# Performance work log

Hardware: AMD Instinct MI355X
Metric: run time of the kernel (lower is better)

The kernel has to match this reference:

```python
import jax, jax.numpy as jnp
import numpy as np

N = 100000; E = 1000000; D = 192; FD = 64; L = 6; MLP = 192
TW = 768; NPD = 6; CPD = 7; TEMP = 0.5; NREL = 2; EPS = 1e-5


def _ln(x, g, b):
    mu = jnp.mean(x, axis=-1, keepdims=True)
    var = jnp.mean(jnp.square(x - mu), axis=-1, keepdims=True)
    return (x - mu) * jax.lax.rsqrt(var + EPS) * g + b


def _bn(x, g, b):
    # BatchNorm1d in training mode: batch statistics over the N (node) axis
    mu = jnp.mean(x, axis=0, keepdims=True)
    var = jnp.mean(jnp.square(x - mu), axis=0, keepdims=True)
    return (x - mu) * jax.lax.rsqrt(var + EPS) * g + b


def _rgcn(x, Wrel, Wroot, bias, src, dst, etype):
    # PyG RGCNConv, aggr='mean': out_i = x_i @ Wroot + b + sum_r mean_{j in N_r(i)} x_j @ W_r
    out = x @ Wroot + bias
    for r in range(NREL):
        h = x @ Wrel[r]                                   # [N, D] per-relation transform
        mask = (etype == r)
        msg = jnp.where(mask[:, None], jnp.take(h, src, axis=0), 0.0)  # [E, D]
        agg = jax.ops.segment_sum(msg, dst, num_segments=N)
        cnt = jax.ops.segment_sum(mask.astype(x.dtype), dst, num_segments=N)
        out = out + agg / jnp.maximum(cnt, 1.0)[:, None]
    return out


def _forward(tweet, num_prop, comments_prop,
             Wt, bt, Wn, bnum, Wc, bc,
             Wv, bv, Wo, bo, ln1_g, ln1_b, bn_g, bn_b,
             W1, b1, W2, b2, ln2_g, ln2_b,
             Wrel, Wroot, rgcn_b, Wm1, bm1, Wm2, bm2, Wm3, bm3,
             edge_index, edge_type, labels, train_idx):
    lrelu = jax.nn.leaky_relu  # negative_slope=0.01, same as torch LeakyReLU default
    t = lrelu(tweet @ Wt + bt)
    n = lrelu(num_prop @ Wn + bnum)
    c = lrelu(comments_prop @ Wc + bc)
    x = jnp.concatenate([t, n, c], axis=1)  # [N, D]; seq dim of size 1 is elided
    for i in range(L):
        # MHA over seq_len=1: softmax over a single key is exactly 1, so
        # attn_out = out_proj(v_proj(x)); Q/K projections have zero effect/grad.
        v = x @ Wv[i] + bv[i]
        x = x + (v @ Wo[i] + bo[i])          # dropout in eval mode = identity
        x = _ln(x, ln1_g[i], ln1_b[i])
        x = _bn(x, bn_g[i], bn_b[i])
        f = lrelu(x @ W1[i] + b1[i]) @ W2[i] + b2[i]
        x = x + f
        x = _ln(x, ln2_g[i], ln2_b[i])
    # supervised contrastive loss on first train_idx nodes (train_idx static int)
    feat = x[:train_idx]
    lab = labels[:train_idx]
    fn = feat / jnp.linalg.norm(feat, axis=-1, keepdims=True)
    sim = (fn @ fn.T) / TEMP                              # [T, T]
    ex = jnp.exp(sim)
    match = (lab[:, None] == lab[None, :]).astype(x.dtype)
    closs = jnp.mean(-jnp.log(jnp.sum(match * ex, axis=1) / jnp.sum(ex, axis=1)))
    # two passes through the SAME (shared-weight) RGCN; dropout(p=0.1) eval = identity
    src, dst = edge_index[0], edge_index[1]
    h = _rgcn(x, Wrel, Wroot, rgcn_b, src, dst, edge_type)
    h = _rgcn(h, Wrel, Wroot, rgcn_b, src, dst, edge_type)
    h = lrelu(h @ Wm1 + bm1)
    h = lrelu(h @ Wm2 + bm2)
    logits = h @ Wm3 + bm3                                # [N, 2]
    return logits, closs


def setup_inputs() -> dict:
    key = jax.random.key(0)
    ks = iter(jax.random.split(key, 64))
    f32 = jnp.float32
    def p(*shape):
        fan_in = shape[-2] if len(shape) >= 2 else shape[-1]
        return jax.random.normal(next(ks), shape, f32) * (1.0 / np.sqrt(fan_in))
    inp = {
        'tweet': jax.random.normal(next(ks), (N, TW), f32),
        'num_prop': jax.random.normal(next(ks), (N, NPD), f32),
        'comments_prop': jax.random.normal(next(ks), (N, CPD), f32),
        'Wt': p(TW, FD), 'bt': jnp.zeros((FD,), f32),
        'Wn': p(NPD, FD), 'bnum': jnp.zeros((FD,), f32),
        'Wc': p(CPD, FD), 'bc': jnp.zeros((FD,), f32),
        'Wv': p(L, D, D), 'bv': jnp.zeros((L, D), f32),
        'Wo': p(L, D, D), 'bo': jnp.zeros((L, D), f32),
        'ln1_g': jnp.ones((L, D), f32), 'ln1_b': jnp.zeros((L, D), f32),
        'bn_g': jnp.ones((L, D), f32), 'bn_b': jnp.zeros((L, D), f32),
        'W1': p(L, D, MLP), 'b1': jnp.zeros((L, MLP), f32),
        'W2': p(L, MLP, D), 'b2': jnp.zeros((L, D), f32),
        'ln2_g': jnp.ones((L, D), f32), 'ln2_b': jnp.zeros((L, D), f32),
        'Wrel': p(NREL, D, D), 'Wroot': p(D, D), 'rgcn_b': jnp.zeros((D,), f32),
        'Wm1': p(D, MLP), 'bm1': jnp.zeros((MLP,), f32),
        'Wm2': p(MLP, D), 'bm2': jnp.zeros((D,), f32),
        'Wm3': p(D, 2), 'bm3': jnp.zeros((2,), f32),
        'edge_index': jax.random.randint(next(ks), (2, E), 0, N, jnp.int32),
        'edge_type': jax.random.randint(next(ks), (E,), 0, NREL, jnp.int32),
        'labels': jax.random.randint(next(ks), (N,), 0, 2, jnp.int32),
        'train_idx': 8192,
    }
    return inp


def reference(tweet, num_prop, comments_prop, Wt, bt, Wn, bnum, Wc, bc,
              Wv, bv, Wo, bo, ln1_g, ln1_b, bn_g, bn_b,
              W1, b1, W2, b2, ln2_g, ln2_b,
              Wrel, Wroot, rgcn_b, Wm1, bm1, Wm2, bm2, Wm3, bm3,
              edge_index, edge_type, labels, train_idx):
    return _forward(tweet, num_prop, comments_prop, Wt, bt, Wn, bnum, Wc, bc,
                    Wv, bv, Wo, bo, ln1_g, ln1_b, bn_g, bn_b,
                    W1, b1, W2, b2, ln2_g, ln2_b,
                    Wrel, Wroot, rgcn_b, Wm1, bm1, Wm2, bm2, Wm3, bm3,
                    edge_index, edge_type, labels, train_idx)
```

## Files before the change

### kernel.cpp

```cpp
#include <hip/hip_runtime.h>

#define NN 100000
#define EE 1000000
#define DDIM 192
#define NLAYER 6
#define TRAIN 8192
#define SLOPE 0.01f
#define EPS_LN 1e-5f
#define TOTSEG (2 * NN)
#define SCAN_NB 98

typedef float f32x4 __attribute__((ext_vector_type(4)));
typedef __bf16 bf16x8 __attribute__((ext_vector_type(8)));
typedef unsigned short ushort_t;
typedef unsigned int uint_t;

__device__ __forceinline__ float lrelu(float v) { return v > 0.0f ? v : SLOPE * v; }

__device__ __forceinline__ ushort_t f2bf(float f) {
    __bf16 h = (__bf16)f;
    return __builtin_bit_cast(ushort_t, h);
}

__device__ __forceinline__ float bf2f(ushort_t b) {
// ... 12 lines not shown
    const float* __restrict__ W2, const float* __restrict__ Wrel,
    const float* __restrict__ Wroot, const float* __restrict__ Wm1,
    const float* __restrict__ Wm2, ushort_t* __restrict__ WTt,
    ushort_t* __restrict__ WTs, ushort_t* __restrict__ WTg)
{
    const int bid = blockIdx.x;
    if (bid < 29 * 144) {
        const int mat = bid / 144;
        const int o = (bid % 144) * 256 + threadIdx.x;
        const float* src;
        if      (mat <  6) src = Wv   + (size_t)mat * 36864;
        else if (mat < 12) src = Wo   + (size_t)(mat - 6)  * 36864;
        else if (mat < 18) src = W1   + (size_t)(mat - 12) * 36864;
        else if (mat < 24) src = W2   + (size_t)(mat - 18) * 36864;
        else if (mat < 26) src = Wrel + (size_t)(mat - 24) * 36864;
        else if (mat == 26) src = Wroot;
        else if (mat == 27) src = Wm1;
        else                src = Wm2;
        const int m = o / 192, k = o - m * 192;
        const ushort_t b = f2bf(src[(size_t)k * 192 + m]);
        if (mat == 24 || mat == 25)
            WTg[(size_t)m * 576 + 192 + (mat - 24) * 192 + k] = b;
        else if (mat == 26)
            WTg[(size_t)m * 576 + k] = b;
        else
            WTs[(size_t)mat * 36864 + o] = b;
    } else {
        const int o = (bid - 29 * 144) * 256 + threadIdx.x;
        const int m = o / 768, k = o - m * 768;
        WTt[o] = f2bf(Wt[(size_t)k * 64 + m]);
    }
}

template <int NFRAG, bool BIAS, bool RELU>
__global__ __launch_bounds__(256) void gemm_mfma(
    const float* __restrict__ A, const ushort_t* __restrict__ WT,
    const float* __restrict__ bias, float* __restrict__ C,
    int n, int K, int ldc)
{
    __shared__ ushort_t As[128 * 32];
    __shared__ ushort_t Ws[NFRAG * 16 * 32];
    const int tid = threadIdx.x;
    const int lane = tid & 63, w = tid >> 6;
    const int quad = lane >> 4, l15 = lane & 15;
    const int row0 = blockIdx.x * 128;

    f32x4 acc[2][NFRAG];
    #pragma unroll
    for (int m = 0; m < 2; ++m)
        #pragma unroll
        for (int nf = 0; nf < NFRAG; ++nf)
            acc[m][nf] = (f32x4){0.f, 0.f, 0.f, 0.f};

    const int srow = tid >> 1, shalf = tid & 1;
    const bool arow_ok = (row0 + srow) < n;
    const float* aptr = A + (size_t)(row0 + srow) * K + shalf * 16;
    const int ktiles = K >> 5;

    float f[16];
    if (arow_ok) {
        const float4* p = (const float4*)aptr;
        #pragma unroll
        for (int i = 0; i < 4; ++i) {
            const float4 t4 = p[i];
            f[i * 4 + 0] = t4.x; f[i * 4 + 1] = t4.y;
            f[i * 4 + 2] = t4.z; f[i * 4 + 3] = t4.w;
        }
    } else {
        #pragma unroll
        for (int i = 0; i < 16; ++i) f[i] = 0.f;
    }

    for (int t = 0; t < ktiles; ++t) {
        const int k0 = t << 5;
        uint_t u[8];
        #pragma unroll
        for (int i = 0; i < 8; ++i)
            u[i] = (uint_t)f2bf(f[2 * i]) | ((uint_t)f2bf(f[2 * i + 1]) << 16);
        uint4* dsta = (uint4*)&As[srow * 32 + shalf * 16];
        dsta[0] = make_uint4(u[0], u[1], u[2], u[3]);
        dsta[1] = make_uint4(u[4], u[5], u[6], u[7]);

        #pragma unroll
        for (int s = tid; s < NFRAG * 64; s += 256) {
            const int col = s >> 2, part = s & 3;
            *(uint4*)&Ws[col * 32 + part * 8] =
                *(const uint4*)(WT + (size_t)col * K + k0 + part * 8);
        }
        __syncthreads();

        float fn_[16];
        const bool more = (t + 1 < ktiles);
        if (more) {
            if (arow_ok) {
                const float4* p = (const float4*)(aptr + k0 + 32);
                #pragma unroll
                for (int i = 0; i < 4; ++i) {
                    const float4 t4 = p[i];
                    fn_[i * 4 + 0] = t4.x; fn_[i * 4 + 1] = t4.y;
                    fn_[i * 4 + 2] = t4.z; fn_[i * 4 + 3] = t4.w;
                }
            } else {
                #pragma unroll
                for (int i = 0; i < 16; ++i) fn_[i] = 0.f;
            }
        }

        const bf16x8 a0 = *(const bf16x8*)&As[(w * 32 + l15) * 32 + quad * 8];
        const bf16x8 a1 = *(const bf16x8*)&As[(w * 32 + 16 + l15) * 32 + quad * 8];
        #pragma unroll
        for (int nf = 0; nf < NFRAG; ++nf) {
            const bf16x8 b = *(const bf16x8*)&Ws[(nf * 16 + l15) * 32 + quad * 8];
            acc[0][nf] = __builtin_amdgcn_mfma_f32_16x16x32_bf16(a0, b, acc[0][nf], 0, 0, 0);
            acc[1][nf] = __builtin_amdgcn_mfma_f32_16x16x32_bf16(a1, b, acc[1][nf], 0, 0, 0);
        }
        __syncthreads();
        if (more) {
            #pragma unroll
            for (int i = 0; i < 16; ++i) f[i] = fn_[i];
        }
    }

    #pragma unroll
    for (int m = 0; m < 2; ++m) {
        #pragma unroll
        for (int reg = 0; reg < 4; ++reg) {
            const int gr = row0 + w * 32 + m * 16 + quad * 4 + reg;
            if (gr >= n) continue;
            #pragma unroll
            for (int nf = 0; nf < NFRAG; ++nf) {
                const int col = nf * 16 + l15;
                float x = acc[m][nf][reg] + (BIAS ? bias[col] : 0.f);
                if (RELU) x = lrelu(x);
                C[(size_t)gr * ldc + col] = x;
            }
        }
    }
}

template <bool ABF, bool RELU1, bool RELU2, bool RES, bool LNORM, bool BN,
          bool BNSTAT, bool CF32, bool CBF>
__global__ __launch_bounds__(512, 4) void gemm2_mfma(
    const void* __restrict__ Ain, const ushort_t* __restrict__ wta,
    const float* __restrict__ bias1, const ushort_t* __restrict__ wtb,
    const float* __restrict__ bias2, const void* __restrict__ resin,
    float* __restrict__ C, ushort_t* __restrict__ Cbf,
    const float* __restrict__ bnsum, const float* __restrict__ bng,
    const float* __restrict__ bnb, float* __restrict__ bnacc,
    const float* __restrict__ lg, const float* __restrict__ lb, int n)
{
    constexpr int VST = 200;
    __shared__ ushort_t Vs[128 * VST];
    __shared__ ushort_t Ws[2][192 * 32];
    __shared__ float scs[DDIM], shs[DDIM];
    const int tid = threadIdx.x;
    const int lane = tid & 63, w = tid >> 6;
    const int quad = lane >> 4, l15 = lane & 15;
    const int row0 = blockIdx.x * 128;
    const int myrow = row0 + w * 16 + l15;
    const bool rok = myrow < n;

    if constexpr (BN) {
        const float invN = 1.0f / (float)NN;
        for (int j = tid; j < DDIM; j += 512) {
            const float mu = bnsum[j] * invN;
            const float var = bnsum[DDIM + j] * invN - mu * mu;
            const float sc = bng[j] * rsqrtf(var + EPS_LN);
            scs[j] = sc;
            shs[j] = fmaf(-mu, sc, bnb[j]);
        }
    }

    f32x4 acc[12];
    #pragma unroll
    for (int nf = 0; nf < 12; ++nf) acc[nf] = (f32x4){0.f, 0.f, 0.f, 0.f};

    const float*    aF = (const float*)Ain    + (size_t)myrow * DDIM + quad * 8;
    const ushort_t* aB = (const ushort_t*)Ain + (size_t)myrow * DDIM + quad * 8;

    auto stageW = [&](const ushort_t* wt, int t, int b) {
        const int k0 = t << 5;
        for (int s = tid; s < 768; s += 512) {
            const int col = s >> 2, part = s & 3;
            *(uint4*)&Ws[b][col * 32 + part * 8] =
                *(const uint4*)(wt + (size_t)col * DDIM + k0 + part * 8);
        }
    };
    auto loadA = [&](int t, float* fo, uint4& uo) {
        if constexpr (!ABF) {
            if (rok) {
                const float4 p0 = *(const float4*)(aF + t * 32);
                const float4 p1 = *(const float4*)(aF + t * 32 + 4);
                fo[0] = p0.x; fo[1] = p0.y; fo[2] = p0.z; fo[3] = p0.w;
                fo[4] = p1.x; fo[5] = p1.y; fo[6] = p1.z; fo[7] = p1.w;
            } else {
                #pragma unroll
                for (int i = 0; i < 8; ++i) fo[i] = 0.f;
            }
        } else {
            uo = rok ? *(const uint4*)(aB + t * 32) : make_uint4(0u, 0u, 0u, 0u);
        }
    };
    auto makeA = [&](const float* fi, const uint4& ui, int t) -> bf16x8 {
        if constexpr (!ABF) {
            union { uint_t u[4]; bf16x8 v; } r;
            #pragma unroll
            for (int i = 0; i < 4; ++i)
                r.u[i] = (uint_t)f2bf(fi[2 * i]) | ((uint_t)f2bf(fi[2 * i + 1]) << 16);
            return r.v;
        } else if constexpr (BN) {
            const int c0 = (t << 5) + quad * 8;
            const float4 sc0 = *(const float4*)&scs[c0];
            const float4 sc1 = *(const float4*)&scs[c0 + 4];
            const float4 sh0 = *(const float4*)&shs[c0];
            const float4 sh1 = *(const float4*)&shs[c0 + 4];
            const uint_t* uw = (const uint_t*)&ui;
            float x[8];
            #pragma unroll
            for (int i = 0; i < 4; ++i) {
                x[2 * i]     = bf2f((ushort_t)(uw[i] & 0xffffu));
                x[2 * i + 1] = bf2f((ushort_t)(uw[i] >> 16));
            }
            x[0] = fmaf(x[0], sc0.x, sh0.x); x[1] = fmaf(x[1], sc0.y, sh0.y);
            x[2] = fmaf(x[2], sc0.z, sh0.z); x[3] = fmaf(x[3], sc0.w, sh0.w);
            x[4] = fmaf(x[4], sc1.x, sh1.x); x[5] = fmaf(x[5], sc1.y, sh1.y);
            x[6] = fmaf(x[6], sc1.z, sh1.z); x[7] = fmaf(x[7], sc1.w, sh1.w);
            union { uint_t u[4]; bf16x8 v; } r;
            #pragma unroll
            for (int i = 0; i < 4; ++i)
                r.u[i] = (uint_t)f2bf(x[2 * i]) | ((uint_t)f2bf(x[2 * i + 1]) << 16);
            return r.v;
        } else {
            return __builtin_bit_cast(bf16x8, ui);
        }
    };

    float fc[8]; uint4 uc;
    stageW(wta, 0, 0);
    loadA(0, fc, uc);
    __syncthreads();
    #pragma unroll 2
    for (int t = 0; t < 6; ++t) {
        const int b = t & 1;
        if (t < 5) stageW(wta, t + 1, b ^ 1);
        float fn[8]; uint4 un;
        if (t < 5) loadA(t + 1, fn, un);
        const bf16x8 a = makeA(fc, uc, t);
        #pragma unroll
        for (int nf = 0; nf < 12; ++nf) {
            const bf16x8 bb = *(const bf16x8*)&Ws[b][(nf * 16 + l15) * 32 + quad * 8];
            acc[nf] = __builtin_amdgcn_mfma_f32_16x16x32_bf16(a, bb, acc[nf], 0, 0, 0);
        }
        __syncthreads();
        if (t < 5) {
            if constexpr (!ABF) {
                #pragma unroll
                for (int i = 0; i < 8; ++i) fc[i] = fn[i];
            } else uc = un;
        }
    }

    {
        float b1r[12];
        #pragma unroll
        for (int nf = 0; nf < 12; ++nf) b1r[nf] = bias1[nf * 16 + l15];
        #pragma unroll
        for (int reg = 0; reg < 4; ++reg) {
            ushort_t* vrow = &Vs[(w * 16 + quad * 4 + reg) * VST + l15];
            #pragma unroll
            for (int nf = 0; nf < 12; ++nf) {
                float x = acc[nf][reg] + b1r[nf];
                if (RELU1) x = lrelu(x);
                vrow[nf * 16] = f2bf(x);
                acc[nf][reg] = 0.f;
            }
        }
    }
    stageW(wtb, 0, 0);
    __syncthreads();

    #pragma unroll 2
    for (int t = 0; t < 6; ++t) {
        const int b = t & 1;
        if (t < 5) stageW(wtb, t + 1, b ^ 1);
        const bf16x8 a = *(const bf16x8*)&Vs[(w * 16 + l15) * VST + (t << 5) + quad * 8];
        #pragma unroll
        for (int nf = 0; nf < 12; ++nf) {
            const bf16x8 bb = *(const bf16x8*)&Ws[b][(nf * 16 + l15) * 32 + quad * 8];
            acc[nf] = __builtin_amdgcn_mfma_f32_16x16x32_bf16(a, bb, acc[nf], 0, 0, 0);
        }
        __syncthreads();
    }

    int   col[12];
    float bia[12];
    #pragma unroll
    for (int nf = 0; nf < 12; ++nf) {
        col[nf] = nf * 16 + l15;
        bia[nf] = bias2[col[nf]];
    }
    float rsc[12], rsh[12];
    if constexpr (BN && RES) {
        #pragma unroll
        for (int nf = 0; nf < 12; ++nf) {
            rsc[nf] = scs[col[nf]];
            rsh[nf] = shs[col[nf]];
        }
    }
    float cs[12], cs2[12];
    if constexpr (BNSTAT) {
        #pragma unroll
        for (int nf = 0; nf < 12; ++nf) { cs[nf] = 0.f; cs2[nf] = 0.f; }
    }
    #pragma unroll
    for (int reg = 0; reg < 4; ++reg) {
        const int gr = row0 + w * 16 + quad * 4 + reg;
        const bool ok = gr < n;
        float v[12];
        #pragma unroll
        for (int nf = 0; nf < 12; ++nf) {
            float x = acc[nf][reg] + bia[nf];
            if constexpr (RES) {
                float r;
                if constexpr (ABF)
                    r = ok ? bf2f(((const ushort_t*)resin)[(size_t)gr * DDIM + col[nf]]) : 0.f;
                else
                    r = ok ? ((const float*)resin)[(size_t)gr * DDIM + col[nf]] : 0.f;
                if constexpr (BN) r = fmaf(r, rsc[nf], rsh[nf]);
                x += r;
            }
            v[nf] = x;
        }
        if constexpr (LNORM) {
            float s = 0.f, s2 = 0.f;
            #pragma unroll
            for (int nf = 0; nf < 12; ++nf) { s += v[nf]; s2 = fmaf(v[nf], v[nf], s2); }
            #pragma unroll
            for (int off = 1; off < 16; off <<= 1) {
                s  += __shfl_xor(s, off);
                s2 += __shfl_xor(s2, off);
            }
            const float mu = s * (1.0f / DDIM);
            const float var = s2 * (1.0f / DDIM) - mu * mu;
            const float rs = rsqrtf(var + EPS_LN);
            #pragma unroll
            for (int nf = 0; nf < 12; ++nf)
                v[nf] = fmaf((v[nf] - mu) * rs, lg[col[nf]], lb[col[nf]]);
        }
        #pragma unroll
        for (int nf = 0; nf < 12; ++nf) {
            float x = v[nf];
            if (RELU2) x = lrelu(x);
            if constexpr (BNSTAT) {
                const float xa = ok ? x : 0.f;
                cs[nf] += xa;
                cs2[nf] = fmaf(xa, xa, cs2[nf]);
            }
            if (ok) {
                if constexpr (CF32) C[(size_t)gr * DDIM + col[nf]] = x;
                if constexpr (CBF)  Cbf[(size_t)gr * DDIM + col[nf]] = f2bf(x);
            }
        }
    }
    if constexpr (BNSTAT) {
        float* bsA = (float*)&Ws[0][0];
        float* bsB = bsA + 8 * 192;
        #pragma unroll
        for (int nf = 0; nf < 12; ++nf) {
            cs[nf]  += __shfl_xor(cs[nf], 16);  cs[nf]  += __shfl_xor(cs[nf], 32);
            cs2[nf] += __shfl_xor(cs2[nf], 16); cs2[nf] += __shfl_xor(cs2[nf], 32);
        }
        if (quad == 0) {
            #pragma unroll
            for (int nf = 0; nf < 12; ++nf) {
                bsA[w * 192 + col[nf]] = cs[nf];
                bsB[w * 192 + col[nf]] = cs2[nf];
            }
        }
        __syncthreads();
        if (tid < DDIM) {
            float s = 0.f, s2 = 0.f;
            #pragma unroll
            for (int k = 0; k < 8; ++k) {
                s  += bsA[k * 192 + tid];
                s2 += bsB[k * 192 + tid];
            }
            atomicAdd(&bnacc[tid], s);
            atomicAdd(&bnacc[DDIM + tid], s2);
        }
    }
}

__global__ __launch_bounds__(512, 4) void gemm_cat(
// ... 37 lines not shown

    #pragma unroll 2
    for (int t = 0; t < 18; ++t) {
        const int b = t & 1;
        if (t < 17) stageW(t + 1, b ^ 1);
        uint4 un;
        if (t < 17) un = loadA(t + 1);
        const bf16x8 a = __builtin_bit_cast(bf16x8, uc);
        #pragma unroll
        for (int nf = 0; nf < 12; ++nf) {
            const bf16x8 bb = *(const bf16x8*)&Ws[b][(nf * 16 + l15) * 32 + quad * 8];
            acc[nf] = __builtin_amdgcn_mfma_f32_16x16x32_bf16(a, bb, acc[nf], 0, 0, 0);
        }
        __syncthreads();
        if (t < 17) uc = un;
    }

    #pragma unroll
    for (int reg = 0; reg < 4; ++reg) {
        const int gr = row0 + w * 16 + quad * 4 + reg;
        if (gr >= n) continue;
        #pragma unroll
        for (int nf = 0; nf < 12; ++nf) {
            const int col = nf * 16 + l15;
            Cbf[(size_t)gr * DDIM + col] = f2bf(acc[nf][reg] + bias[col]);
        }
    }
}

__global__ __launch_bounds__(256) void embed_nc_k(
    const float* __restrict__ np_, const float* __restrict__ cp,
    const float* __restrict__ Wn, const float* __restrict__ bnum,
    const float* __restrict__ Wc, const float* __restrict__ bc,
    float* __restrict__ x)
{
    const int idx = blockIdx.x * 256 + threadIdx.x;
    if (idx >= NN * 128) return;
    const int node = idx >> 7;
    const int c = idx & 127;
    float acc;
    if (c < 64) {
        acc = bnum[c];
        #pragma unroll
        for (int k = 0; k < 6; ++k) acc = fmaf(np_[node * 6 + k], Wn[k * 64 + c], acc);
    } else {
        const int cc = c - 64;
        acc = bc[cc];
        #pragma unroll
        for (int k = 0; k < 7; ++k) acc = fmaf(cp[node * 7 + k], Wc[k * 64 + cc], acc);
    }
    x[(size_t)node * DDIM + 64 + c] = lrelu(acc);
}

__global__ __launch_bounds__(256) void fnorm_k(const float* __restrict__ x,
                                               ushort_t* __restrict__ fnb)
{
    const int wave = threadIdx.x >> 6, lane = threadIdx.x & 63;
    const int row = blockIdx.x * 4 + wave;
    if (row >= TRAIN) return;
    const float* xr = x + (size_t)row * DDIM;
    const float v0 = xr[lane], v1 = xr[lane + 64], v2 = xr[lane + 128];
    const float q = wave_sum(v0 * v0 + v1 * v1 + v2 * v2);
    const float inv = 1.0f / sqrtf(q);
    ushort_t* fr = fnb + (size_t)row * DDIM;
    fr[lane]       = f2bf(v0 * inv);
    fr[lane + 64]  = f2bf(v1 * inv);
    fr[lane + 128] = f2bf(v2 * inv);
}

__global__ __launch_bounds__(256) void sim_mfma(const ushort_t* __restrict__ fnb,
    const int* __restrict__ lab, float* __restrict__ row_ex, float* __restrict__ row_mt)
{
    __shared__ ushort_t Ai[128 * 32];
    __shared__ ushort_t Bj[128 * 32];
    __shared__ int Li[128], Lj[128];
    const int tid = threadIdx.x, lane = tid & 63, w = tid >> 6;
    const int quad = lane >> 4, l15 = lane & 15;
    const int i0 = blockIdx.x * 128, j0 = blockIdx.y * 128;
    if (tid < 128) Li[tid] = lab[i0 + tid];
    else           Lj[tid - 128] = lab[j0 + tid - 128];
    const int iw = (w >> 1) * 64, jw = (w & 1) * 64;

    f32x4 acc[4][4];
    #pragma unroll
    for (int m = 0; m < 4; ++m)
        #pragma unroll
        for (int nf = 0; nf < 4; ++nf)
            acc[m][nf] = (f32x4){0.f, 0.f, 0.f, 0.f};

    for (int k0 = 0; k0 < DDIM; k0 += 32) {
        #pragma unroll
        for (int s = tid; s < 512; s += 256) {
            const int row = s >> 2, part = s & 3;
            *(uint4*)&Ai[row * 32 + part * 8] =
                *(const uint4*)(fnb + (size_t)(i0 + row) * DDIM + k0 + part * 8);
            *(uint4*)&Bj[row * 32 + part * 8] =
                *(const uint4*)(fnb + (size_t)(j0 + row) * DDIM + k0 + part * 8);
        }
        __syncthreads();
        bf16x8 a[4], b[4];
        #pragma unroll
        for (int m = 0; m < 4; ++m)
            a[m] = *(const bf16x8*)&Ai[(iw + m * 16 + l15) * 32 + quad * 8];
        #pragma unroll
        for (int nf = 0; nf < 4; ++nf)
            b[nf] = *(const bf16x8*)&Bj[(jw + nf * 16 + l15) * 32 + quad * 8];
        #pragma unroll
        for (int m = 0; m < 4; ++m)
            #pragma unroll
            for (int nf = 0; nf < 4; ++nf)
                acc[m][nf] = __builtin_amdgcn_mfma_f32_16x16x32_bf16(a[m], b[nf], acc[m][nf], 0, 0, 0);
        __syncthreads();
    }

    int lj[4];
    #pragma unroll
    for (int nf = 0; nf < 4; ++nf) lj[nf] = Lj[jw + nf * 16 + l15];
    #pragma unroll
    for (int m = 0; m < 4; ++m) {
        #pragma unroll
        for (int reg = 0; reg < 4; ++reg) {
            const int rl = iw + m * 16 + quad * 4 + reg;
            const int li = Li[rl];
            float se = 0.f, sm = 0.f;
            #pragma unroll
            for (int nf = 0; nf < 4; ++nf) {
                const float e = __expf(acc[m][nf][reg] * 2.0f);
                se += e;
                if (li == lj[nf]) sm += e;
            }
            #pragma unroll
            for (int off = 1; off < 16; off <<= 1) {
                se += __shfl_xor(se, off);
                sm += __shfl_xor(sm, off);
            }
            if (l15 == 0) {
                atomicAdd(&row_ex[i0 + rl], se);
                atomicAdd(&row_mt[i0 + rl], sm);
            }
        }
    }
}

__global__ __launch_bounds__(256) void closs_k(const float* __restrict__ ex,
    const float* __restrict__ mt, float* __restrict__ out)
{
    float s = 0.f;
    for (int i = threadIdx.x; i < TRAIN; i += 256) s += -logf(mt[i] / ex[i]);
    s = wave_sum(s);
    __shared__ float red[4];
    const int wave = threadIdx.x >> 6, lane = threadIdx.x & 63;
    if (lane == 0) red[wave] = s;
    __syncthreads();
    if (threadIdx.x == 0) out[0] = (red[0] + red[1] + red[2] + red[3]) / (float)TRAIN;
}

__global__ __launch_bounds__(256) void cnt_i_k(const int* __restrict__ dst,
    const int* __restrict__ ety, int* __restrict__ cnti)
{
    const int e = blockIdx.x * 256 + threadIdx.x;
    if (e >= EE) return;
    atomicAdd(&cnti[(size_t)ety[e] * NN + dst[e]], 1);
}

__global__ __launch_bounds__(256) void part_k(const int* __restrict__ cnti,
                                              int* __restrict__ part)
{
    __shared__ int sh[256];
    const int tid = threadIdx.x;
    const int i0 = blockIdx.x * 2048 + tid * 8;
    int s = 0;
// ... 84 lines not shown
        const int seg = r * NN + d;
        const int end = offs[seg];
        const int c = cnti[seg];
        float a0 = 0.f, a1 = 0.f, b0 = 0.f, b1 = 0.f;
        int e = end - c;
        for (; e + 1 < end; e += 2) {
            const int s0 = elist[e], s1 = elist[e + 1];
            const uint_t* r0 = (const uint_t*)(xb + (size_t)s0 * DDIM);
            const uint_t* r1 = (const uint_t*)(xb + (size_t)s1 * DDIM);
            const uint_t x0 = r0[lane], x1 = r1[lane];
            uint_t y0 = 0u, y1 = 0u;
            if (lo) { y0 = r0[64 + lane]; y1 = r1[64 + lane]; }
            a0 += bf2f((ushort_t)(x0 & 0xffffu)) + bf2f((ushort_t)(x1 & 0xffffu));
            a1 += bf2f((ushort_t)(x0 >> 16))     + bf2f((ushort_t)(x1 >> 16));
            b0 += bf2f((ushort_t)(y0 & 0xffffu)) + bf2f((ushort_t)(y1 & 0xffffu));
            b1 += bf2f((ushort_t)(y0 >> 16))     + bf2f((ushort_t)(y1 >> 16));
        }
        if (e < end) {
            const int s0 = elist[e];
            const uint_t* r0 = (const uint_t*)(xb + (size_t)s0 * DDIM);
            const uint_t x0 = r0[lane];
            uint_t y0 = 0u;
            if (lo) y0 = r0[64 + lane];
            a0 += bf2f((ushort_t)(x0 & 0xffffu));
            a1 += bf2f((ushort_t)(x0 >> 16));
            b0 += bf2f((ushort_t)(y0 & 0xffffu));
            b1 += bf2f((ushort_t)(y0 >> 16));
        }
        const float inv = 1.0f / (float)max(c, 1);
        uint_t* ar = (uint_t*)(aggb + (size_t)d * 384 + r * DDIM);
        ar[lane] = (uint_t)f2bf(a0 * inv) | ((uint_t)f2bf(a1 * inv) << 16);
        if (lo)
            ar[64 + lane] = (uint_t)f2bf(b0 * inv) | ((uint_t)f2bf(b1 * inv) << 16);
    }
}

__global__ __launch_bounds__(256) void logits_k(const float* __restrict__ h,
    const float* __restrict__ Wm3, const float* __restrict__ bm3, float* __restrict__ out)
{
    const int wave = threadIdx.x >> 6, lane = threadIdx.x & 63;
    const int row = blockIdx.x * 4 + wave;
    if (row >= NN) return;
    const float* hr = h + (size_t)row * DDIM;
    float s0 = 0.f, s1 = 0.f;
    #pragma unroll
    for (int p = 0; p < 3; ++p) {
        const int k = lane + p * 64;
        const float v = hr[k];
        s0 = fmaf(v, Wm3[k * 2 + 0], s0);
        s1 = fmaf(v, Wm3[k * 2 + 1], s1);
    }
    #pragma unroll
    for (int off = 32; off > 0; off >>= 1) {
        s0 += __shfl_down(s0, off);
        s1 += __shfl_down(s1, off);
    }
    if (lane == 0) {
        out[(size_t)row * 2 + 0] = s0 + bm3[0];
        out[(size_t)row * 2 + 1] = s1 + bm3[1];
    }
}

extern "C" void kernel_launch(void* const* d_in, const int* in_sizes, int n_in,
                              void* d_out, int out_size, void* d_ws, size_t ws_size,
                              hipStream_t stream)
{
    const float* tweet   = (const float*)d_in[0];
    const float* np_     = (const float*)d_in[1];
    const float* cp      = (const float*)d_in[2];
    const float* Wt      = (const float*)d_in[3];
    const float* bt      = (const float*)d_in[4];
    const float* Wn      = (const float*)d_in[5];
    const float* bnum    = (const float*)d_in[6];
    const float* Wc      = (const float*)d_in[7];
    const float* bc      = (const float*)d_in[8];
    const float* Wv      = (const float*)d_in[9];
    const float* bv      = (const float*)d_in[10];
    const float* Wo      = (const float*)d_in[11];
    const float* bo      = (const float*)d_in[12];
    const float* ln1g    = (const float*)d_in[13];
    const float* ln1b    = (const float*)d_in[14];
    const float* bng     = (const float*)d_in[15];
    const float* bnb     = (const float*)d_in[16];
    const float* W1      = (const float*)d_in[17];
    const float* b1      = (const float*)d_in[18];
    const float* W2      = (const float*)d_in[19];
    const float* b2      = (const float*)d_in[20];
    const float* ln2g    = (const float*)d_in[21];
    const float* ln2b    = (const float*)d_in[22];
    const float* Wrel    = (const float*)d_in[23];
    const float* Wroot   = (const float*)d_in[24];
    const float* rgcnb   = (const float*)d_in[25];
    const float* Wm1     = (const float*)d_in[26];
    const float* bm1     = (const float*)d_in[27];
    const float* Wm2     = (const float*)d_in[28];
    const float* bm2     = (const float*)d_in[29];
    const float* Wm3     = (const float*)d_in[30];
    const float* bm3     = (const float*)d_in[31];
    const int*   eidx    = (const int*)d_in[32];
    const int*   esrc    = eidx;
    const int*   edst    = eidx + EE;
    const int*   ety     = (const int*)d_in[33];
    const int*   labels  = (const int*)d_in[34];
    float* out = (float*)d_out;

    float* ws = (float*)d_ws;
    const size_t ND = (size_t)NN * DDIM;
    float* B0    = ws;
    float* B1    = B0 + ND;
    float* B2    = B1 + ND;
    float* B3    = B2 + ND;
    float* ROWEX = B3 + ND;
    float* ROWMT = ROWEX + TRAIN;
    float* BNS   = ROWMT + TRAIN;
    int*   CNTI  = (int*)(BNS + 12 * DDIM);
    int*   OFFS  = CNTI + 2 * NN;
    int*   ELIST = OFFS + 2 * NN;
    int*   PART  = ELIST + EE;
    ushort_t* FNb = (ushort_t*)(PART + 128);
    ushort_t* WTt = FNb + (size_t)TRAIN * DDIM;
    ushort_t* WTs = WTt + 49152;
    ushort_t* WTv    = WTs;
    ushort_t* WTo    = WTs + (size_t)6  * 36864;
    ushort_t* WT1    = WTs + (size_t)12 * 36864;
    ushort_t* WT2    = WTs + (size_t)18 * 36864;
    ushort_t* WTm1   = WTs + (size_t)27 * 36864;
    ushort_t* WTm2   = WTs + (size_t)28 * 36864;
    ushort_t* XBF  = (ushort_t*)B3;
    ushort_t* WTg  = (ushort_t*)B3 + ND;
    ushort_t* X1BF = (ushort_t*)B2;
    ushort_t* AGGB = (ushort_t*)B2;

    const int gx = (NN + 127) / 128;
    const dim3 blk(256);
    const dim3 blk5(512);

    prep_w<<<29 * 144 + 192, blk, 0, stream>>>(Wt, Wv, Wo, W1, W2, Wrel, Wroot, Wm1, Wm2, WTt, WTs, WTg);

    hipMemsetAsync(CNTI, 0, 2 * NN * sizeof(int), stream);
    cnt_i_k<<<(EE + 255) / 256, blk, 0, stream>>>(edst, ety, CNTI);
    part_k<<<SCAN_NB, blk, 0, stream>>>(CNTI, PART);
    scanp_k<<<1, 128, 0, stream>>>(PART);
    offs_k<<<SCAN_NB, blk, 0, stream>>>(CNTI, PART, OFFS);
    fill_k<<<(EE + 255) / 256, blk, 0, stream>>>(esrc, edst, ety, OFFS, ELIST);

    gemm_mfma<4, true, true><<<gx, blk, 0, stream>>>(tweet, WTt, bt, B0, NN, 768, DDIM);
    embed_nc_k<<<(NN * 128 + 255) / 256, blk, 0, stream>>>(np_, cp, Wn, bnum, Wc, bc, B0);

    hipMemsetAsync(BNS, 0, 12 * DDIM * sizeof(float), stream);
    for (int i = 0; i < NLAYER; ++i) {
        const size_t wo = (size_t)i * 36864;
        float* bnacc_i = BNS + (size_t)i * 2 * DDIM;
        gemm2_mfma<false, false, false, true, true, false, true, false, true>
            <<<gx, blk5, 0, stream>>>(
            B0, WTv + wo, bv + i * DDIM, WTo + wo, bo + i * DDIM, B0,
            nullptr, X1BF, nullptr, nullptr, nullptr, bnacc_i,
            ln1g + i * DDIM, ln1b + i * DDIM, NN);
        if (i < NLAYER - 1)
            gemm2_mfma<true, true, false, true, true, true, false, true, false>
                <<<gx, blk5, 0, stream>>>(
                X1BF, WT1 + wo, b1 + i * DDIM, WT2 + wo, b2 + i * DDIM, X1BF,
                B0, nullptr, bnacc_i, bng + i * DDIM, bnb + i * DDIM, nullptr,
                ln2g + i * DDIM, ln2b + i * DDIM, NN);
        else
            gemm2_mfma<true, true, false, true, true, true, false, true, true>
                <<<gx, blk5, 0, stream>>>(
                X1BF, WT1 + wo, b1 + i * DDIM, WT2 + wo, b2 + i * DDIM, X1BF,
                B0, XBF, bnacc_i, bng + i * DDIM, bnb + i * DDIM, nullptr,
                ln2g + i * DDIM, ln2b + i * DDIM, NN);
    }

    hipMemsetAsync(ROWEX, 0, 2 * TRAIN * sizeof(float), stream);
    fnorm_k<<<TRAIN / 4, blk, 0, stream>>>(B0, FNb);
    sim_mfma<<<dim3(TRAIN / 128, TRAIN / 128), blk, 0, stream>>>(FNb, labels, ROWEX, ROWMT);
    closs_k<<<1, blk, 0, stream>>>(ROWEX, ROWMT, out + 2 * (size_t)NN);

    gather_bf_k<<<(NN + 3) / 4, blk, 0, stream>>>(XBF, ELIST, OFFS, CNTI, AGGB);
    gemm_cat<<<gx, blk5, 0, stream>>>(XBF, AGGB, WTg, rgcnb, XBF, NN);

    gather_bf_k<<<(NN + 3) / 4, blk, 0, stream>>>(XBF, ELIST, OFFS, CNTI, AGGB);
    gemm_cat<<<gx, blk5, 0, stream>>>(XBF, AGGB, WTg, rgcnb, XBF, NN);

    gemm2_mfma<true, true, true, false, false, false, false, true, false>
        <<<gx, blk5, 0, stream>>>(
        XBF, WTm1, bm1, WTm2, bm2, nullptr, B2, nullptr,
        nullptr, nullptr, nullptr, nullptr, nullptr, nullptr, NN);
    logits_k<<<(NN + 3) / 4, blk, 0, stream>>>(B2, Wm3, bm3, out);
}
```

Baseline: 1.894 ms.

## Store activations in bf16 and fuse logits, fnorm, and symmetric similarity

The residual stream is now kept entirely in bf16: the tweet embedding GEMM and the layer GEMMs write bf16 instead of fp32, which roughly halves activation traffic. The logits head is fused into the final MLP GEMM epilogue, and feature normalisation is fused into the last layer's epilogue. The similarity kernel now computes only the lower-triangular tiles and adds each off-diagonal tile's contributions to both rows and columns, halving its MFMA work at the cost of extra atomics. The tweet GEMM is rewritten with 512 threads and a double-buffered weight tile. Keeping the residual in bf16 adds rounding error at every layer.

New measurement: 1.852 ms. 1.02x faster.

```diff
diff --git a/kernel.cpp b/kernel.cpp
--- a/kernel.cpp
+++ b/kernel.cpp
@@ -68,122 +68,93 @@
     }
 }
 
-template <int NFRAG, bool BIAS, bool RELU>
-__global__ __launch_bounds__(256) void gemm_mfma(
+__global__ __launch_bounds__(512) void gemm_tweet(
     const float* __restrict__ A, const ushort_t* __restrict__ WT,
-    const float* __restrict__ bias, float* __restrict__ C,
-    int n, int K, int ldc)
-{
-    __shared__ ushort_t As[128 * 32];
-    __shared__ ushort_t Ws[NFRAG * 16 * 32];
+    const float* __restrict__ bias, ushort_t* __restrict__ Cbf, int n)
+{
+    __shared__ ushort_t Ws[2][64 * 32];
     const int tid = threadIdx.x;
     const int lane = tid & 63, w = tid >> 6;
     const int quad = lane >> 4, l15 = lane & 15;
     const int row0 = blockIdx.x * 128;
-
-    f32x4 acc[2][NFRAG];
-    #pragma unroll
-    for (int m = 0; m < 2; ++m)
-        #pragma unroll
-        for (int nf = 0; nf < NFRAG; ++nf)
-            acc[m][nf] = (f32x4){0.f, 0.f, 0.f, 0.f};
-
-    const int srow = tid >> 1, shalf = tid & 1;
-    const bool arow_ok = (row0 + srow) < n;
-    const float* aptr = A + (size_t)(row0 + srow) * K + shalf * 16;
-    const int ktiles = K >> 5;
-
-    float f[16];
-    if (arow_ok) {
-        const float4* p = (const float4*)aptr;
-        #pragma unroll
-        for (int i = 0; i < 4; ++i) {
-            const float4 t4 = p[i];
-            f[i * 4 + 0] = t4.x; f[i * 4 + 1] = t4.y;
-            f[i * 4 + 2] = t4.z; f[i * 4 + 3] = t4.w;
-        }
-    } else {
-        #pragma unroll
-        for (int i = 0; i < 16; ++i) f[i] = 0.f;
-    }
-
-    for (int t = 0; t < ktiles; ++t) {
-        const int k0 = t << 5;
-        uint_t u[8];
-        #pragma unroll
-        for (int i = 0; i < 8; ++i)
-            u[i] = (uint_t)f2bf(f[2 * i]) | ((uint_t)f2bf(f[2 * i + 1]) << 16);
-        uint4* dsta = (uint4*)&As[srow * 32 + shalf * 16];
-        dsta[0] = make_uint4(u[0], u[1], u[2], u[3]);
-        dsta[1] = make_uint4(u[4], u[5], u[6], u[7]);
-
-        #pragma unroll
-        for (int s = tid; s < NFRAG * 64; s += 256) {
-            const int col = s >> 2, part = s & 3;
-            *(uint4*)&Ws[col * 32 + part * 8] =
-                *(const uint4*)(WT + (size_t)col * K + k0 + part * 8);
-        }
-        __syncthreads();
-
-        float fn_[16];
-        const bool more = (t + 1 < ktiles);
-        if (more) {
-            if (arow_ok) {
-                const float4* p = (const float4*)(aptr + k0 + 32);
-                #pragma unroll
-                for (int i = 0; i < 4; ++i) {
-                    const float4 t4 = p[i];
-                    fn_[i * 4 + 0] = t4.x; fn_[i * 4 + 1] = t4.y;
-                    fn_[i * 4 + 2] = t4.z; fn_[i * 4 + 3] = t4.w;
-                }
-            } else {
-                #pragma unroll
-                for (int i = 0; i < 16; ++i) fn_[i] = 0.f;
-            }
-        }
-
-        const bf16x8 a0 = *(const bf16x8*)&As[(w * 32 + l15) * 32 + quad * 8];
-        const bf16x8 a1 = *(const bf16x8*)&As[(w * 32 + 16 + l15) * 32 + quad * 8];
-        #pragma unroll
-        for (int nf = 0; nf < NFRAG; ++nf) {
-            const bf16x8 b = *(const bf16x8*)&Ws[(nf * 16 + l15) * 32 + quad * 8];
-            acc[0][nf] = __builtin_amdgcn_mfma_f32_16x16x32_bf16(a0, b, acc[0][nf], 0, 0, 0);
-            acc[1][nf] = __builtin_amdgcn_mfma_f32_16x16x32_bf16(a1, b, acc[1][nf], 0, 0, 0);
-        }
-        __syncthreads();
-        if (more) {
-            #pragma unroll
-            for (int i = 0; i < 16; ++i) f[i] = fn_[i];
-        }
-    }
-
-    #pragma unroll
-    for (int m = 0; m < 2; ++m) {
-        #pragma unroll
-        for (int reg = 0; reg < 4; ++reg) {
-            const int gr = row0 + w * 32 + m * 16 + quad * 4 + reg;
-            if (gr >= n) continue;
-            #pragma unroll
-            for (int nf = 0; nf < NFRAG; ++nf) {
-                const int col = nf * 16 + l15;
-                float x = acc[m][nf][reg] + (BIAS ? bias[col] : 0.f);
-                if (RELU) x = lrelu(x);
-                C[(size_t)gr * ldc + col] = x;
-            }
-        }
-    }
-}
-
-template <bool ABF, bool RELU1, bool RELU2, bool RES, bool LNORM, bool BN,
-          bool BNSTAT, bool CF32, bool CBF>
+    const int myrow = row0 + w * 16 + l15;
+    const bool rok = myrow < n;
+
+    f32x4 acc[4];
+    #pragma unroll
+    for (int nf = 0; nf < 4; ++nf) acc[nf] = (f32x4){0.f, 0.f, 0.f, 0.f};
+
+    const float* aF = A + (size_t)myrow * 768 + quad * 8;
+
+    auto stageW = [&](int t, int b) {
+        if (tid < 256) {
+            const int col = tid >> 2, part = tid & 3;
+            *(uint4*)&Ws[b][col * 32 + part * 8] =
+                *(const uint4*)(WT + (size_t)col * 768 + (t << 5) + part * 8);
+        }
+    };
+    auto loadA = [&](int t, float* fo) {
+        if (rok) {
+            const float4 p0 = *(const float4*)(aF + t * 32);
+            const float4 p1 = *(const float4*)(aF + t * 32 + 4);
+            fo[0] = p0.x; fo[1] = p0.y; fo[2] = p0.z; fo[3] = p0.w;
+            fo[4] = p1.x; fo[5] = p1.y; fo[6] = p1.z; fo[7] = p1.w;
+        } else {
+            #pragma unroll
+            for (int i = 0; i < 8; ++i) fo[i] = 0.f;
+        }
+    };
+
+    float fc[8];
+    stageW(0, 0);
+    loadA(0, fc);
+    __syncthreads();
+    #pragma unroll 2
+    for (int t = 0; t < 24; ++t) {
+        const int b = t & 1;
+        if (t < 23) stageW(t + 1, b ^ 1);
+        float fn[8];
+        if (t < 23) loadA(t + 1, fn);
+        union { uint_t u[4]; bf16x8 v; } r;
+        #pragma unroll
+        for (int i = 0; i < 4; ++i)
+            r.u[i] = (uint_t)f2bf(fc[2 * i]) | ((uint_t)f2bf(fc[2 * i + 1]) << 16);
+        #pragma unroll
+        for (int nf = 0; nf < 4; ++nf) {
+            const bf16x8 bb = *(const bf16x8*)&Ws[b][(nf * 16 + l15) * 32 + quad * 8];
+            acc[nf] = __builtin_amdgcn_mfma_f32_16x16x32_bf16(r.v, bb, acc[nf], 0, 0, 0);
+        }
+        __syncthreads();
+        if (t < 23) {
+            #pragma unroll
+            for (int i = 0; i < 8; ++i) fc[i] = fn[i];
+        }
+    }
+
+    #pragma unroll
+    for (int reg = 0; reg < 4; ++reg) {
+        const int gr = row0 + w * 16 + quad * 4 + reg;
+        if (gr >= n) continue;
+        #pragma unroll
+        for (int nf = 0; nf < 4; ++nf) {
+            const int col = nf * 16 + l15;
+            Cbf[(size_t)gr * DDIM + col] = f2bf(lrelu(acc[nf][reg] + bias[col]));
+        }
+    }
+}
+
+template <bool RELU1, bool RELU2, bool RES, bool LNORM, bool BN,
+          bool BNSTAT, bool CBF, bool LOGITS, bool FNORM>
 __global__ __launch_bounds__(512, 4) void gemm2_mfma(
-    const void* __restrict__ Ain, const ushort_t* __restrict__ wta,
+    const ushort_t* __restrict__ Ain, const ushort_t* __restrict__ wta,
     const float* __restrict__ bias1, const ushort_t* __restrict__ wtb,
-    const float* __restrict__ bias2, const void* __restrict__ resin,
-    float* __restrict__ C, ushort_t* __restrict__ Cbf,
+    const float* __restrict__ bias2, const ushort_t* __restrict__ resin,
+    ushort_t* __restrict__ Cbf,
     const float* __restrict__ bnsum, const float* __restrict__ bng,
     const float* __restrict__ bnb, float* __restrict__ bnacc,
-    const float* __restrict__ lg, const float* __restrict__ lb, int n)
+    const float* __restrict__ lg, const float* __restrict__ lb,
+    const float* __restrict__ Wm3, const float* __restrict__ bm3,
+    float* __restrict__ outp, ushort_t* __restrict__ fnb, int n)
 {
     constexpr int VST = 200;
     __shared__ ushort_t Vs[128 * VST];
@@ -211,8 +182,7 @@
     #pragma unroll
     for (int nf = 0; nf < 12; ++nf) acc[nf] = (f32x4){0.f, 0.f, 0.f, 0.f};
 
-    const float*    aF = (const float*)Ain    + (size_t)myrow * DDIM + quad * 8;
-    const ushort_t* aB = (const ushort_t*)Ain + (size_t)myrow * DDIM + quad * 8;
+    const ushort_t* aB = Ain + (size_t)myrow * DDIM + quad * 8;
 
     auto stageW = [&](const ushort_t* wt, int t, int b) {
         const int k0 = t << 5;
@@ -222,29 +192,11 @@
                 *(const uint4*)(wt + (size_t)col * DDIM + k0 + part * 8);
         }
     };
-    auto loadA = [&](int t, float* fo, uint4& uo) {
-        if constexpr (!ABF) {
-            if (rok) {
-                const float4 p0 = *(const float4*)(aF + t * 32);
-                const float4 p1 = *(const float4*)(aF + t * 32 + 4);
-                fo[0] = p0.x; fo[1] = p0.y; fo[2] = p0.z; fo[3] = p0.w;
-                fo[4] = p1.x; fo[5] = p1.y; fo[6] = p1.z; fo[7] = p1.w;
-            } else {
-                #pragma unroll
-                for (int i = 0; i < 8; ++i) fo[i] = 0.f;
-            }
-        } else {
-            uo = rok ? *(const uint4*)(aB + t * 32) : make_uint4(0u, 0u, 0u, 0u);
-        }
+    auto loadA = [&](int t) -> uint4 {
+        return rok ? *(const uint4*)(aB + t * 32) : make_uint4(0u, 0u, 0u, 0u);
     };
-    auto makeA = [&](const float* fi, const uint4& ui, int t) -> bf16x8 {
-        if constexpr (!ABF) {
-            union { uint_t u[4]; bf16x8 v; } r;
-            #pragma unroll
-            for (int i = 0; i < 4; ++i)
-                r.u[i] = (uint_t)f2bf(fi[2 * i]) | ((uint_t)f2bf(fi[2 * i + 1]) << 16);
-            return r.v;
-        } else if constexpr (BN) {
+    auto makeA = [&](const uint4& ui, int t) -> bf16x8 {
+        if constexpr (BN) {
             const int c0 = (t << 5) + quad * 8;
             const float4 sc0 = *(const float4*)&scs[c0];
             const float4 sc1 = *(const float4*)&scs[c0 + 4];
@@ -271,29 +223,24 @@
         }
     };
 
-    float fc[8]; uint4 uc;
+    uint4 uc;
     stageW(wta, 0, 0);
-    loadA(0, fc, uc);
+    uc = loadA(0);
     __syncthreads();
     #pragma unroll 2
     for (int t = 0; t < 6; ++t) {
         const int b = t & 1;
         if (t < 5) stageW(wta, t + 1, b ^ 1);
-        float fn[8]; uint4 un;
-        if (t < 5) loadA(t + 1, fn, un);
-        const bf16x8 a = makeA(fc, uc, t);
+        uint4 un;
+        if (t < 5) un = loadA(t + 1);
+        const bf16x8 a = makeA(uc, t);
         #pragma unroll
         for (int nf = 0; nf < 12; ++nf) {
             const bf16x8 bb = *(const bf16x8*)&Ws[b][(nf * 16 + l15) * 32 + quad * 8];
             acc[nf] = __builtin_amdgcn_mfma_f32_16x16x32_bf16(a, bb, acc[nf], 0, 0, 0);
         }
         __syncthreads();
-        if (t < 5) {
-            if constexpr (!ABF) {
-                #pragma unroll
-                for (int i = 0; i < 8; ++i) fc[i] = fn[i];
-            } else uc = un;
-        }
+        if (t < 5) uc = un;
     }
 
     {
@@ -343,6 +290,14 @@
             rsh[nf] = shs[col[nf]];
         }
     }
+    float w3a[12], w3b[12];
+    if constexpr (LOGITS) {
+        #pragma unroll
+        for (int nf = 0; nf < 12; ++nf) {
+            w3a[nf] = Wm3[col[nf] * 2 + 0];
+            w3b[nf] = Wm3[col[nf] * 2 + 1];
+        }
+    }
     float cs[12], cs2[12];
     if constexpr (BNSTAT) {
         #pragma unroll
@@ -357,11 +312,7 @@
         for (int nf = 0; nf < 12; ++nf) {
             float x = acc[nf][reg] + bia[nf];
             if constexpr (RES) {
-                float r;
-                if constexpr (ABF)
-                    r = ok ? bf2f(((const ushort_t*)resin)[(size_t)gr * DDIM + col[nf]]) : 0.f;
-                else
-                    r = ok ? ((const float*)resin)[(size_t)gr * DDIM + col[nf]] : 0.f;
+                float r = ok ? bf2f(resin[(size_t)gr * DDIM + col[nf]]) : 0.f;
                 if constexpr (BN) r = fmaf(r, rsc[nf], rsh[nf]);
                 x += r;
             }
@@ -383,6 +334,7 @@
             for (int nf = 0; nf < 12; ++nf)
                 v[nf] = fmaf((v[nf] - mu) * rs, lg[col[nf]], lb[col[nf]]);
         }
+        float s0 = 0.f, s1 = 0.f;
         #pragma unroll
         for (int nf = 0; nf < 12; ++nf) {
             float x = v[nf];
@@ -392,9 +344,36 @@
                 cs[nf] += xa;
                 cs2[nf] = fmaf(xa, xa, cs2[nf]);
             }
+            if constexpr (LOGITS) {
+                s0 = fmaf(x, w3a[nf], s0);
+                s1 = fmaf(x, w3b[nf], s1);
+            }
             if (ok) {
-                if constexpr (CF32) C[(size_t)gr * DDIM + col[nf]] = x;
-                if constexpr (CBF)  Cbf[(size_t)gr * DDIM + col[nf]] = f2bf(x);
+                if constexpr (CBF) Cbf[(size_t)gr * DDIM + col[nf]] = f2bf(x);
+            }
+        }
+        if constexpr (LOGITS) {
+            #pragma unroll
+            for (int off = 1; off < 16; off <<= 1) {
+                s0 += __shfl_xor(s0, off);
+                s1 += __shfl_xor(s1, off);
+            }
+            if (l15 == 0 && ok) {
+                outp[(size_t)gr * 2 + 0] = s0 + bm3[0];
+                outp[(size_t)gr * 2 + 1] = s1 + bm3[1];
+            }
+        }
+        if constexpr (FNORM) {
+            if (gr < TRAIN) {
+                float q = 0.f;
+                #pragma unroll
+                for (int nf = 0; nf < 12; ++nf) q = fmaf(v[nf], v[nf], q);
+                #pragma unroll
+                for (int off = 1; off < 16; off <<= 1) q += __shfl_xor(q, off);
+                const float inv = 1.0f / sqrtf(q);
+                #pragma unroll
+                for (int nf = 0; nf < 12; ++nf)
+                    fnb[(size_t)gr * DDIM + col[nf]] = f2bf(v[nf] * inv);
             }
         }
     }
@@ -498,7 +477,7 @@
     const float* __restrict__ np_, const float* __restrict__ cp,
     const float* __restrict__ Wn, const float* __restrict__ bnum,
     const float* __restrict__ Wc, const float* __restrict__ bc,
-    float* __restrict__ x)
+    ushort_t* __restrict__ xb)
 {
     const int idx = blockIdx.x * 256 + threadIdx.x;
     if (idx >= NN * 128) return;
@@ -515,23 +494,7 @@
         #pragma unroll
         for (int k = 0; k < 7; ++k) acc = fmaf(cp[node * 7 + k], Wc[k * 64 + cc], acc);
     }
-    x[(size_t)node * DDIM + 64 + c] = lrelu(acc);
-}
-
-__global__ __launch_bounds__(256) void fnorm_k(const float* __restrict__ x,
-                                               ushort_t* __restrict__ fnb)
-{
-    const int wave = threadIdx.x >> 6, lane = threadIdx.x & 63;
-    const int row = blockIdx.x * 4 + wave;
-    if (row >= TRAIN) return;
-    const float* xr = x + (size_t)row * DDIM;
-    const float v0 = xr[lane], v1 = xr[lane + 64], v2 = xr[lane + 128];
-    const float q = wave_sum(v0 * v0 + v1 * v1 + v2 * v2);
-    const float inv = 1.0f / sqrtf(q);
-    ushort_t* fr = fnb + (size_t)row * DDIM;
-    fr[lane]       = f2bf(v0 * inv);
-    fr[lane + 64]  = f2bf(v1 * inv);
-    fr[lane + 128] = f2bf(v2 * inv);
+    xb[(size_t)node * DDIM + 64 + c] = f2bf(lrelu(acc));
 }
 
 __global__ __launch_bounds__(256) void sim_mfma(const ushort_t* __restrict__ fnb,
@@ -540,9 +503,16 @@
     __shared__ ushort_t Ai[128 * 32];
     __shared__ ushort_t Bj[128 * 32];
     __shared__ int Li[128], Lj[128];
+    const int bid = blockIdx.x;
+    int ti = (int)((sqrtf(8.0f * (float)bid + 1.0f) - 1.0f) * 0.5f);
+    while ((ti + 1) * (ti + 2) / 2 <= bid) ++ti;
+    while (ti * (ti + 1) / 2 > bid) --ti;
+    const int tj = bid - ti * (ti + 1) / 2;
+    const int i0 = ti * 128, j0 = tj * 128;
+    const bool offd = (ti != tj);
+
     const int tid = threadIdx.x, lane = tid & 63, w = tid >> 6;
     const int quad = lane >> 4, l15 = lane & 15;
-    const int i0 = blockIdx.x * 128, j0 = blockIdx.y * 128;
     if (tid < 128) Li[tid] = lab[i0 + tid];
     else           Lj[tid - 128] = lab[j0 + tid - 128];
     const int iw = (w >> 1) * 64, jw = (w & 1) * 64;
@@ -582,6 +552,10 @@
     int lj[4];
     #pragma unroll
     for (int nf = 0; nf < 4; ++nf) lj[nf] = Lj[jw + nf * 16 + l15];
+    float ce[4], cm[4];
+    #pragma unroll
+    for (int nf = 0; nf < 4; ++nf) { ce[nf] = 0.f; cm[nf] = 0.f; }
+
     #pragma unroll
     for (int m = 0; m < 4; ++m) {
         #pragma unroll
@@ -593,7 +567,12 @@
             for (int nf = 0; nf < 4; ++nf) {
                 const float e = __expf(acc[m][nf][reg] * 2.0f);
                 se += e;
-                if (li == lj[nf]) sm += e;
+                const bool mt = (li == lj[nf]);
+                if (mt) sm += e;
+                if (offd) {
+                    ce[nf] += e;
+                    if (mt) cm[nf] += e;
+                }
             }
             #pragma unroll
             for (int off = 1; off < 16; off <<= 1) {
@@ -603,6 +582,20 @@
             if (l15 == 0) {
                 atomicAdd(&row_ex[i0 + rl], se);
                 atomicAdd(&row_mt[i0 + rl], sm);
+            }
+        }
+    }
+    if (offd) {
+        #pragma unroll
+        for (int nf = 0; nf < 4; ++nf) {
+            ce[nf] += __shfl_xor(ce[nf], 16); ce[nf] += __shfl_xor(ce[nf], 32);
+            cm[nf] += __shfl_xor(cm[nf], 16); cm[nf] += __shfl_xor(cm[nf], 32);
+        }
+        if (quad == 0) {
+            #pragma unroll
+            for (int nf = 0; nf < 4; ++nf) {
+                atomicAdd(&row_ex[j0 + jw + nf * 16 + l15], ce[nf]);
+                atomicAdd(&row_mt[j0 + jw + nf * 16 + l15], cm[nf]);
             }
         }
     }
@@ -753,32 +746,6 @@
         ar[lane] = (uint_t)f2bf(a0 * inv) | ((uint_t)f2bf(a1 * inv) << 16);
         if (lo)
             ar[64 + lane] = (uint_t)f2bf(b0 * inv) | ((uint_t)f2bf(b1 * inv) << 16);
-    }
-}
-
-__global__ __launch_bounds__(256) void logits_k(const float* __restrict__ h,
-    const float* __restrict__ Wm3, const float* __restrict__ bm3, float* __restrict__ out)
-{
-    const int wave = threadIdx.x >> 6, lane = threadIdx.x & 63;
-    const int row = blockIdx.x * 4 + wave;
-    if (row >= NN) return;
-    const float* hr = h + (size_t)row * DDIM;
-    float s0 = 0.f, s1 = 0.f;
-    #pragma unroll
-    for (int p = 0; p < 3; ++p) {
-        const int k = lane + p * 64;
-        const float v = hr[k];
-        s0 = fmaf(v, Wm3[k * 2 + 0], s0);
-        s1 = fmaf(v, Wm3[k * 2 + 1], s1);
-    }
-    #pragma unroll
-    for (int off = 32; off > 0; off >>= 1) {
-        s0 += __shfl_down(s0, off);
-        s1 += __shfl_down(s1, off);
-    }
-    if (lane == 0) {
-        out[(size_t)row * 2 + 0] = s0 + bm3[0];
-        out[(size_t)row * 2 + 1] = s1 + bm3[1];
     }
 }
 
@@ -825,32 +792,27 @@
     const int*   labels  = (const int*)d_in[34];
     float* out = (float*)d_out;
 
-    float* ws = (float*)d_ws;
     const size_t ND = (size_t)NN * DDIM;
-    float* B0    = ws;
-    float* B1    = B0 + ND;
-    float* B2    = B1 + ND;
-    float* B3    = B2 + ND;
-    float* ROWEX = B3 + ND;
+    ushort_t* XBF  = (ushort_t*)d_ws;
+    ushort_t* X1BF = XBF + ND;
+    ushort_t* AGGB = X1BF + ND;
+    ushort_t* FNb  = AGGB + 2 * ND;
+    ushort_t* WTt  = FNb + (size_t)TRAIN * DDIM;
+    ushort_t* WTs  = WTt + 49152;
+    ushort_t* WTg  = WTs + (size_t)29 * 36864;
+    float* ROWEX = (float*)(WTg + 110592);
     float* ROWMT = ROWEX + TRAIN;
     float* BNS   = ROWMT + TRAIN;
     int*   CNTI  = (int*)(BNS + 12 * DDIM);
     int*   OFFS  = CNTI + 2 * NN;
     int*   ELIST = OFFS + 2 * NN;
     int*   PART  = ELIST + EE;
-    ushort_t* FNb = (ushort_t*)(PART + 128);
-    ushort_t* WTt = FNb + (size_t)TRAIN * DDIM;
-    ushort_t* WTs = WTt + 49152;
-    ushort_t* WTv    = WTs;
-    ushort_t* WTo    = WTs + (size_t)6  * 36864;
-    ushort_t* WT1    = WTs + (size_t)12 * 36864;
-    ushort_t* WT2    = WTs + (size_t)18 * 36864;
-    ushort_t* WTm1   = WTs + (size_t)27 * 36864;
-    ushort_t* WTm2   = WTs + (size_t)28 * 36864;
-    ushort_t* XBF  = (ushort_t*)B3;
-    ushort_t* WTg  = (ushort_t*)B3 + ND;
-    ushort_t* X1BF = (ushort_t*)B2;
-    ushort_t* AGGB = (ushort_t*)B2;
+    ushort_t* WTv  = WTs;
+    ushort_t* WTo  = WTs + (size_t)6  * 36864;
+    ushort_t* WT1  = WTs + (size_t)12 * 36864;
+    ushort_t* WT2  = WTs + (size_t)18 * 36864;
+    ushort_t* WTm1 = WTs + (size_t)27 * 36864;
+    ushort_t* WTm2 = WTs + (size_t)28 * 36864;
 
     const int gx = (NN + 127) / 128;
     const dim3 blk(256);
@@ -865,35 +827,34 @@
     offs_k<<<SCAN_NB, blk, 0, stream>>>(CNTI, PART, OFFS);
     fill_k<<<(EE + 255) / 256, blk, 0, stream>>>(esrc, edst, ety, OFFS, ELIST);
 
-    gemm_mfma<4, true, true><<<gx, blk, 0, stream>>>(tweet, WTt, bt, B0, NN, 768, DDIM);
-    embed_nc_k<<<(NN * 128 + 255) / 256, blk, 0, stream>>>(np_, cp, Wn, bnum, Wc, bc, B0);
+    gemm_tweet<<<gx, blk5, 0, stream>>>(tweet, WTt, bt, XBF, NN);
+    embed_nc_k<<<(NN * 128 + 255) / 256, blk, 0, stream>>>(np_, cp, Wn, bnum, Wc, bc, XBF);
 
     hipMemsetAsync(BNS, 0, 12 * DDIM * sizeof(float), stream);
     for (int i = 0; i < NLAYER; ++i) {
         const size_t wo = (size_t)i * 36864;
         float* bnacc_i = BNS + (size_t)i * 2 * DDIM;
-        gemm2_mfma<false, false, false, true, true, false, true, false, true>
+        gemm2_mfma<false, false, true, true, false, true, true, false, false>
             <<<gx, blk5, 0, stream>>>(
-            B0, WTv + wo, bv + i * DDIM, WTo + wo, bo + i * DDIM, B0,
-            nullptr, X1BF, nullptr, nullptr, nullptr, bnacc_i,
-            ln1g + i * DDIM, ln1b + i * DDIM, NN);
+            XBF, WTv + wo, bv + i * DDIM, WTo + wo, bo + i * DDIM, XBF,
+            X1BF, nullptr, nullptr, nullptr, bnacc_i,
+            ln1g + i * DDIM, ln1b + i * DDIM, nullptr, nullptr, nullptr, nullptr, NN);
         if (i < NLAYER - 1)
-            gemm2_mfma<true, true, false, true, true, true, false, true, false>
+            gemm2_mfma<true, false, true, true, true, false, true, false, false>
                 <<<gx, blk5, 0, stream>>>(
                 X1BF, WT1 + wo, b1 + i * DDIM, WT2 + wo, b2 + i * DDIM, X1BF,
-                B0, nullptr, bnacc_i, bng + i * DDIM, bnb + i * DDIM, nullptr,
-                ln2g + i * DDIM, ln2b + i * DDIM, NN);
+                XBF, bnacc_i, bng + i * DDIM, bnb + i * DDIM, nullptr,
+                ln2g + i * DDIM, ln2b + i * DDIM, nullptr, nullptr, nullptr, nullptr, NN);
         else
-            gemm2_mfma<true, true, false, true, true, true, false, true, true>
+            gemm2_mfma<true, false, true, true, true, false, true, false, true>
                 <<<gx, blk5, 0, stream>>>(
                 X1BF, WT1 + wo, b1 + i * DDIM, WT2 + wo, b2 + i * DDIM, X1BF,
-                B0, XBF, bnacc_i, bng + i * DDIM, bnb + i * DDIM, nullptr,
-                ln2g + i * DDIM, ln2b + i * DDIM, NN);
+                XBF, bnacc_i, bng + i * DDIM, bnb + i * DDIM, nullptr,
+                ln2g + i * DDIM, ln2b + i * DDIM, nullptr, nullptr, nullptr, FNb, NN);
     }
 
     hipMemsetAsync(ROWEX, 0, 2 * TRAIN * sizeof(float), stream);
-    fnorm_k<<<TRAIN / 4, blk, 0, stream>>>(B0, FNb);
-    sim_mfma<<<dim3(TRAIN / 128, TRAIN / 128), blk, 0, stream>>>(FNb, labels, ROWEX, ROWMT);
+    sim_mfma<<<(TRAIN / 128) * (TRAIN / 128 + 1) / 2, blk, 0, stream>>>(FNb, labels, ROWEX, ROWMT);
     closs_k<<<1, blk, 0, stream>>>(ROWEX, ROWMT, out + 2 * (size_t)NN);
 
     gather_bf_k<<<(NN + 3) / 4, blk, 0, stream>>>(XBF, ELIST, OFFS, CNTI, AGGB);
@@ -902,9 +863,9 @@
     gather_bf_k<<<(NN + 3) / 4, blk, 0, stream>>>(XBF, ELIST, OFFS, CNTI, AGGB);
     gemm_cat<<<gx, blk5, 0, stream>>>(XBF, AGGB, WTg, rgcnb, XBF, NN);
 
-    gemm2_mfma<true, true, true, false, false, false, false, true, false>
+    gemm2_mfma<true, true, false, false, false, false, false, true, false>
         <<<gx, blk5, 0, stream>>>(
-        XBF, WTm1, bm1, WTm2, bm2, nullptr, B2, nullptr,
-        nullptr, nullptr, nullptr, nullptr, nullptr, nullptr, NN);
-    logits_k<<<(NN + 3) / 4, blk, 0, stream>>>(B2, Wm3, bm3, out);
-}
+        XBF, WTm1, bm1, WTm2, bm2, nullptr, nullptr,
+        nullptr, nullptr, nullptr, nullptr, nullptr, nullptr,
+        Wm3, bm3, out, nullptr, NN);
+}
```
